# Optimization experiments

Measured on AMD Instinct MI355X. Metric: run time of the kernel, lower is better.

The kernel has to match this reference:

```python
import jax, jax.numpy as jnp
import numpy as np
import math

B, S, E, H = 2, 2048, 1024, 16
D = E // H
EPS = 1e-5


def setup_inputs() -> dict:
    key = jax.random.key(0)
    ks = jax.random.split(key, 6)
    s = 1.0 / math.sqrt(E)
    return {
        "query": jax.random.normal(ks[0], (B, S, E), jnp.float32),
        "Wq": jax.random.normal(ks[1], (E, E), jnp.float32) * s,
        "bq": jnp.zeros((E,), jnp.float32),
        "Wk": jax.random.normal(ks[2], (E, E), jnp.float32) * s,
        "bk": jnp.zeros((E,), jnp.float32),
        "Wv": jax.random.normal(ks[3], (E, E), jnp.float32) * s,
        "bv": jnp.zeros((E,), jnp.float32),
        "Wo": jax.random.normal(ks[4], (E, E), jnp.float32) * s,
        "bo": jnp.zeros((E,), jnp.float32),
        "alpha": jnp.ones((1,), jnp.float32),
    }


def reference(query, Wq, bq, Wk, bk, Wv, bv, Wo, bo, alpha):
    # Q/K/V projections (nn.Linear: x @ W.T + b)
    q = (query @ Wq.T + bq).reshape(B, S, H, D)
    k = (query @ Wk.T + bk).reshape(B, S, H, D)
    v = (query @ Wv.T + bv).reshape(B, S, H, D)

    # YAT scores: (q.k)^2 / (||q-k||^2 + eps)
    qk = jnp.einsum('bqhd,bkhd->bhqk', q, k)          # [B,H,S,S]
    sq = jnp.einsum('bqhd,bqhd->bhq', q, q)           # ||q||^2
    sk = jnp.einsum('bkhd,bkhd->bhk', k, k)           # ||k||^2
    dist_sq = sq[..., :, None] + sk[..., None, :] - 2.0 * qk
    scores = (qk * qk) / (dist_sq + EPS)

    # learnable alpha scaling: scores * (sqrt(d)/log(1+d))^alpha
    scale = (jnp.sqrt(jnp.float32(D)) / jnp.log1p(jnp.float32(D))) ** alpha[0]
    scores = scores * scale

    attn = jax.nn.softmax(scores, axis=-1)
    out = jnp.einsum('bhqk,bkhd->bqhd', attn, v).reshape(B, S, E)
    return out @ Wo.T + bo
```

## Files before the change

kernel.cpp:

```cpp
#include <hip/hip_runtime.h>
#include <hip/hip_fp16.h>
#include <math.h>

#define BB 2
#define SS 2048
#define EE 1024
#define HH 16
#define DD 64
#define YAT_EPS 1e-5f
#define RR (BB * HH * SS)

typedef __attribute__((ext_vector_type(8))) short bf16x8;
typedef __attribute__((ext_vector_type(4))) short short4v;
typedef __attribute__((ext_vector_type(4))) float f32x4;
#define MFMA16(a, b, c) __builtin_amdgcn_mfma_f32_16x16x32_bf16((a), (b), (c), 0, 0, 0)

#if __has_builtin(__builtin_amdgcn_exp2f)
#define EXP2(x) __builtin_amdgcn_exp2f(x)
#else
#define EXP2(x) exp2f(x)
#endif
#if __has_builtin(__builtin_amdgcn_rcpf)
#define RCPF(x) __builtin_amdgcn_rcpf(x)
#else
#define RCPF(x) (1.0f / (x))
#endif

__device__ __forceinline__ unsigned short f2bf(float x) {
    unsigned int u = __float_as_uint(x);
    u += 0x7FFFu + ((u >> 16) & 1u);
    return (unsigned short)(u >> 16);
}
__device__ __forceinline__ float bf2f(unsigned short h) {
    return __uint_as_float(((unsigned int)h) << 16);
}
__device__ __forceinline__ short f2bf_t(float x) {
    return (short)(__float_as_uint(x) >> 16);
}

__device__ __forceinline__ void async_ld16(void* lds, const void* g) {
    __builtin_amdgcn_global_load_lds(
        (const __attribute__((address_space(1))) unsigned int*)g,
        (__attribute__((address_space(3))) unsigned int*)lds, 16, 0, 0);
}

__global__ __launch_bounds__(256) void split_f32(const float* __restrict__ in,
                                                 unsigned short* __restrict__ hi,
                                                 unsigned short* __restrict__ lo,
                                                 int n4) {
    int i = blockIdx.x * 256 + threadIdx.x;
    if (i >= n4) return;
    float4 v = ((const float4*)in)[i];
    ushort4 h, l;
    h.x = f2bf(v.x); l.x = f2bf(v.x - bf2f(h.x));
    h.y = f2bf(v.y); l.y = f2bf(v.y - bf2f(h.y));
    h.z = f2bf(v.z); l.z = f2bf(v.z - bf2f(h.z));
    h.w = f2bf(v.w); l.w = f2bf(v.w - bf2f(h.w));
    ((ushort4*)hi)[i] = h;
    ((ushort4*)lo)[i] = l;
}

__global__ __launch_bounds__(256) void split_w4(
        const float* __restrict__ Wq, const float* __restrict__ Wk,
        const float* __restrict__ Wv, const float* __restrict__ Wo,
        unsigned short* __restrict__ Whi, unsigned short* __restrict__ Wlo,
        unsigned short* __restrict__ Wohi) {
    int i = blockIdx.x * 256 + threadIdx.x;
    int y = blockIdx.y;
    const float* src = y == 0 ? Wq : y == 1 ? Wk : y == 2 ? Wv : Wo;
    unsigned short* hi = y < 3 ? Whi + (size_t)y * EE * EE : Wohi;
    float4 v = ((const float4*)src)[i];
    ushort4 h;
    h.x = f2bf(v.x); h.y = f2bf(v.y); h.z = f2bf(v.z); h.w = f2bf(v.w);
    ((ushort4*)hi)[i] = h;
    if (y < 2) {
        unsigned short* lo = Wlo + (size_t)y * EE * EE;
        ushort4 l;
        l.x = f2bf(v.x - bf2f(h.x));
        l.y = f2bf(v.y - bf2f(h.y));
        l.z = f2bf(v.z - bf2f(h.z));
        l.w = f2bf(v.w - bf2f(h.w));
        ((ushort4*)lo)[i] = l;
    }
}

template <int MODE, int PASSES>
__global__ __launch_bounds__(256, 2) void gemm3p(
        const unsigned short* __restrict__ Ahi, const unsigned short* __restrict__ Alo,
        const unsigned short* __restrict__ Bhi, const unsigned short* __restrict__ Blo,
        const float* __restrict__ bq, const float* __restrict__ bk,
        const float* __restrict__ bv,
        float* __restrict__ Cf,
        unsigned short* __restrict__ qhi, unsigned short* __restrict__ qlo,
        unsigned short* __restrict__ khi,
        unsigned short* __restrict__ v_sd,
        float* __restrict__ sqn, float* __restrict__ skn,
        int M, int N, int K) {
    __shared__ __align__(16) unsigned short LA_hi[128 * 32];
    __shared__ __align__(16) unsigned short LA_lo[128 * 32];
    __shared__ __align__(16) unsigned short LB_hi[128 * 32];
    __shared__ __align__(16) unsigned short LB_lo[128 * 32];

    const int t = threadIdx.x;
    const int w = t >> 6, lane = t & 63;
    const int quad = lane >> 4, lr = lane & 15;
    const int wy = w & 1, wx = w >> 1;
    const int m0 = blockIdx.y * 128, n0 = blockIdx.x * 128;

    const unsigned short* gsrc = nullptr;
    unsigned short* ldst = nullptr;
    if (w == 0)      { gsrc = Ahi + (size_t)m0 * K; ldst = LA_hi; }
    else if (w == 2) { gsrc = Bhi + (size_t)n0 * K; ldst = LB_hi; }
    else if (PASSES == 3 && w == 1) { gsrc = Alo + (size_t)m0 * K; ldst = LA_lo; }
    else if (PASSES == 3 && w == 3) { gsrc = Blo + (size_t)n0 * K; ldst = LB_lo; }
    const unsigned short* gl = gsrc ? gsrc + (size_t)(lane >> 2) * K + (lane & 3) * 8
                                    : nullptr;

    f32x4 acc[4][4];
    #pragma unroll
    for (int i = 0; i < 4; ++i)
        #pragma unroll
        for (int j = 0; j < 4; ++j)
            acc[i][j] = (f32x4){0.f, 0.f, 0.f, 0.f};

    for (int k0 = 0; k0 < K; k0 += 32) {
        __syncthreads();
        if (gl) {
            #pragma unroll
            for (int i = 0; i < 8; ++i)
                async_ld16(ldst + i * 512, gl + (size_t)i * 16 * K + k0);
        }
        __syncthreads();
        bf16x8 ah[4], al[4], bh_[4], bl_[4];
        #pragma unroll
        for (int i = 0; i < 4; ++i) {
            ah[i]  = *(const bf16x8*)&LA_hi[(wy * 64 + i * 16 + lr) * 32 + quad * 8];
            bh_[i] = *(const bf16x8*)&LB_hi[(wx * 64 + i * 16 + lr) * 32 + quad * 8];
            if (PASSES == 3) {
                al[i]  = *(const bf16x8*)&LA_lo[(wy * 64 + i * 16 + lr) * 32 + quad * 8];
                bl_[i] = *(const bf16x8*)&LB_lo[(wx * 64 + i * 16 + lr) * 32 + quad * 8];
            }
        }
        #pragma unroll
        for (int mg = 0; mg < 4; ++mg)
            #pragma unroll
            for (int ns = 0; ns < 4; ++ns) {
                f32x4 a = acc[mg][ns];
                a = MFMA16(ah[mg], bh_[ns], a);
                if (PASSES == 3) {
                    a = MFMA16(ah[mg], bl_[ns], a);
                    a = MFMA16(al[mg], bh_[ns], a);
                }
                acc[mg][ns] = a;
            }
    }

    const int ng = n0 + wx * 64;
    if (MODE == 0) {
        float bias_v[4];
        #pragma unroll
        for (int ns = 0; ns < 4; ++ns) bias_v[ns] = bq[ng + ns * 16 + lr];
        #pragma unroll
        for (int mg = 0; mg < 4; ++mg)
            #pragma unroll
            for (int r = 0; r < 4; ++r) {
                int m = m0 + wy * 64 + mg * 16 + quad * 4 + r;
                #pragma unroll
                for (int ns = 0; ns < 4; ++ns)
                    Cf[(size_t)m * N + ng + ns * 16 + lr] = acc[mg][ns][r] + bias_v[ns];
            }
    } else {
        const int path = MODE == 1 ? (ng >> 10) : 2;
        const int c = MODE == 1 ? (ng & 1023) : ng;
        const int h = c >> 6;
        const float* bias = path == 0 ? bq : path == 1 ? bk : bv;
        unsigned short* hi_p = path == 0 ? qhi : path == 1 ? khi : v_sd;
        float* nrm = path == 0 ? sqn : skn;
        float bias_v[4];
        #pragma unroll
        for (int ns = 0; ns < 4; ++ns) bias_v[ns] = bias[c + ns * 16 + lr];
        #pragma unroll
        for (int mg = 0; mg < 4; ++mg)
            #pragma unroll
            for (int r = 0; r < 4; ++r) {
                int m = m0 + wy * 64 + mg * 16 + quad * 4 + r;
                int b = m >> 11, s = m & (SS - 1);
                size_t base = ((size_t)(b * HH + h) * SS + s) * DD;
                float v4[4];
                #pragma unroll
                for (int ns = 0; ns < 4; ++ns) v4[ns] = acc[mg][ns][r] + bias_v[ns];
                if (path < 2) {
                    float pn = v4[0] * v4[0] + v4[1] * v4[1] + v4[2] * v4[2] + v4[3] * v4[3];
                    #pragma unroll
                    for (int off = 1; off < 16; off <<= 1) pn += __shfl_xor(pn, off);
                    if (lr == 0) nrm[(size_t)(b * HH + h) * SS + s] = pn;
                    #pragma unroll
                    for (int ns = 0; ns < 4; ++ns) {
                        unsigned short hv = f2bf(v4[ns]);
                        hi_p[base + ns * 16 + lr] = hv;
                        if (path == 0)
                            qlo[base + ns * 16 + lr] = f2bf(v4[ns] - bf2f(hv));
                    }
                } else {
                    #pragma unroll
                    for (int ns = 0; ns < 4; ++ns)
                        hi_p[base + ns * 16 + lr] = f2bf(v4[ns]);
                }
            }
    }
}

__global__ __launch_bounds__(256) void transpose_v(const unsigned short* __restrict__ v_sd,
                                                   unsigned short* __restrict__ vt) {
    __shared__ unsigned short T[64][65];
    const int t = threadIdx.x;
    const int bh = blockIdx.y, s0 = blockIdx.x * 64;
    {
        int sl = t >> 2, d4 = (t & 3) * 16;
        const unsigned short* src = &v_sd[((size_t)bh * SS + s0 + sl) * DD + d4];
        bf16x8 a = *(const bf16x8*)src;
        bf16x8 b = *(const bf16x8*)(src + 8);
        #pragma unroll
        for (int j = 0; j < 8; ++j) {
            T[sl][d4 + j] = (unsigned short)a[j];
            T[sl][d4 + 8 + j] = (unsigned short)b[j];
        }
    }
    __syncthreads();
    {
        int dl = t >> 2, s4 = (t & 3) * 16;
        bf16x8 a, b;
        #pragma unroll
        for (int j = 0; j < 8; ++j) {
            a[j] = (short)T[s4 + j][dl];
            b[j] = (short)T[s4 + 8 + j][dl];
        }
        unsigned short* dst = &vt[((size_t)bh * DD + dl) * SS + s0 + s4];
        *(bf16x8*)dst = a;
        *(bf16x8*)(dst + 8) = b;
    }
}

__global__ __launch_bounds__(256, 3) void yat_attn_mfma(
        const unsigned short* __restrict__ qhi, const unsigned short* __restrict__ qlo,
        const unsigned short* __restrict__ khi,
        const unsigned short* __restrict__ vt,
        const float* __restrict__ sqn, const float* __restrict__ skn,
        const float* __restrict__ alphap,
        __half* __restrict__ Opart, float2* __restrict__ mlpart) {
    __shared__ __align__(16) unsigned short Ks[2][4096];
    __shared__ __align__(16) unsigned short Ps[2][4][16 * 68];

    const int t = threadIdx.x;
    const int w = t >> 6, lane = t & 63;
    const int quad = lane >> 4, lr = lane & 15;
    const int qt = blockIdx.x, bh = blockIdx.y, z = blockIdx.z;
    const int row0 = qt * 64 + w * 16;
    const float cscale = powf(sqrtf((float)DD) / log1pf((float)DD), alphap[0])
                         * 1.4426950408889634f;

    bf16x8 qh[2], ql[2];
    #pragma unroll
    for (int kd = 0; kd < 2; ++kd) {
        size_t o = ((size_t)bh * SS + row0 + lr) * DD + kd * 32 + quad * 8;
        qh[kd] = *(const bf16x8*)&qhi[o];
        ql[kd] = *(const bf16x8*)&qlo[o];
    }
    const float sqe = sqn[(size_t)bh * SS + row0 + lr] + YAT_EPS;

    const int lrow = lane >> 3;
    const int lofs = lrow * 64 + (((lane & 7) ^ (lrow & 7)) << 3);

    float m_r = -INFINITY, l_r = 0.f;
    f32x4 O[4];
    #pragma unroll
    for (int nd = 0; nd < 4; ++nd) O[nd] = (f32x4){0.f, 0.f, 0.f, 0.f};

    const int kt0 = z * 16;
    {
        const size_t gbase = ((size_t)bh * SS + kt0 * 64 + w * 16) * 64 + lofs;
        #pragma unroll
        for (int i2 = 0; i2 < 2; ++i2)
            async_ld16(&Ks[0][w * 1024 + i2 * 512], khi + gbase + i2 * 512);
    }

    for (int it = 0; it < 16; ++it) {
        const int kt = kt0 + it;
        const int p = it & 1;
        const int kbase = kt * 64;
        __syncthreads();
        if (it < 15) {
            const size_t gbase = ((size_t)bh * SS + (kt + 1) * 64 + w * 16) * 64 + lofs;
            #pragma unroll
            for (int i2 = 0; i2 < 2; ++i2)
                async_ld16(&Ks[p ^ 1][w * 1024 + i2 * 512], khi + gbase + i2 * 512);
        }
        f32x4 acc[4];
        f32x4 sk4[4];
        const unsigned short* kb = Ks[p];
        const int sw = lr & 7;
        #pragma unroll
        for (int st = 0; st < 4; ++st) {
            const int rbase = (st * 16 + lr) * 64;
            bf16x8 kh0 = *(const bf16x8*)&kb[rbase + ((quad    ) ^ sw) * 8];
            bf16x8 kh1 = *(const bf16x8*)&kb[rbase + ((quad + 4) ^ sw) * 8];
            sk4[st] = *(const f32x4*)&skn[(size_t)bh * SS + kbase + st * 16 + quad * 4];
            f32x4 a = (f32x4){0.f, 0.f, 0.f, 0.f};
            a = MFMA16(kh0, qh[0], a);
            a = MFMA16(kh1, qh[1], a);
            a = MFMA16(kh0, ql[0], a);
            a = MFMA16(kh1, ql[1], a);
            acc[st] = a;
        }
        bf16x8 vf[4][2];
        #pragma unroll
        for (int nd = 0; nd < 4; ++nd)
            #pragma unroll
            for (int kk = 0; kk < 2; ++kk)
                vf[nd][kk] = *(const bf16x8*)&vt[((size_t)bh * DD + nd * 16 + lr) * SS
                                                 + kbase + kk * 32 + quad * 8];
        unsigned short* myP = Ps[p][w];
        float mx = -INFINITY;
        #pragma unroll
        for (int st = 0; st < 4; ++st)
            #pragma unroll
            for (int r = 0; r < 4; ++r) {
                float qk = acc[st][r];
                float d = sqe + sk4[st][r] - 2.f * qk;
                float s = qk * qk * cscale * RCPF(d);
                acc[st][r] = s;
                mx = fmaxf(mx, s);
            }
        mx = fmaxf(mx, __shfl_xor(mx, 16));
        mx = fmaxf(mx, __shfl_xor(mx, 32));
        float mnew = fmaxf(m_r, mx);
        float aa = EXP2(m_r - mnew);
        m_r = mnew;
        float rs = 0.f;
        #pragma unroll
        for (int st = 0; st < 4; ++st)
            #pragma unroll
            for (int r = 0; r < 4; ++r) {
                float e = EXP2(acc[st][r] - mnew);
                acc[st][r] = e;
                rs += e;
            }
        rs += __shfl_xor(rs, 16);
        rs += __shfl_xor(rs, 32);
        l_r = l_r * aa + rs;
        #pragma unroll
        for (int st = 0; st < 4; ++st) {
            short4v pv;
            pv[0] = f2bf_t(acc[st][0]);
            pv[1] = f2bf_t(acc[st][1]);
            pv[2] = f2bf_t(acc[st][2]);
            pv[3] = f2bf_t(acc[st][3]);
            *(short4v*)&myP[lr * 68 + st * 16 + quad * 4] = pv;
        }
        float al_[4];
        #pragma unroll
        for (int r = 0; r < 4; ++r) al_[r] = __shfl(aa, quad * 4 + r);
        #pragma unroll
        for (int nd = 0; nd < 4; ++nd)
            #pragma unroll
            for (int r = 0; r < 4; ++r)
                O[nd][r] *= al_[r];
        bf16x8 pf[2];
        #pragma unroll
        for (int kk = 0; kk < 2; ++kk)
            pf[kk] = *(const bf16x8*)&myP[lr * 68 + kk * 32 + quad * 8];
        #pragma unroll
        for (int nd = 0; nd < 4; ++nd)
            #pragma unroll
            for (int kk = 0; kk < 2; ++kk)
                O[nd] = MFMA16(pf[kk], vf[nd][kk], O[nd]);
    }
    if (quad == 0)
        mlpart[(size_t)z * RR + (size_t)bh * SS + row0 + lr] = make_float2(m_r, l_r);
    #pragma unroll
    for (int r = 0; r < 4; ++r) {
        size_t rowg = (size_t)bh * SS + row0 + quad * 4 + r;
        #pragma unroll
        for (int nd = 0; nd < 4; ++nd)
            Opart[((size_t)z * RR + rowg) * DD + nd * 16 + lr] =
                __float2half(O[nd][r]);
    }
}

__global__ __launch_bounds__(256) void combine_attn(
        const __half* __restrict__ Opart, const float2* __restrict__ mlpart,
        unsigned short* __restrict__ ctxhi) {
    int tid = blockIdx.x * 256 + threadIdx.x;
    int row = tid >> 4, c4 = (tid & 15) * 4;
    float2 ml0 = mlpart[row];
    float2 ml1 = mlpart[RR + row];
    float ms = fmaxf(ml0.x, ml1.x);
    float a0 = EXP2(ml0.x - ms), a1 = EXP2(ml1.x - ms);
    float inv = RCPF(ml0.y * a0 + ml1.y * a1);
    a0 *= inv; a1 *= inv;
    const __half* p0 = Opart + (size_t)row * DD + c4;
    const __half* p1 = p0 + (size_t)RR * DD;
    int bh = row >> 11, s = row & (SS - 1);
    int b = bh >> 4, h = bh & 15;
    size_t idx = ((size_t)b * SS + s) * EE + h * DD + c4;
    ushort4 hv;
    unsigned short* hp = (unsigned short*)&hv;
    #pragma unroll
    for (int j = 0; j < 4; ++j) {
        float o = __half2float(p0[j]) * a0 + __half2float(p1[j]) * a1;
        hp[j] = f2bf(o);
    }
    *(ushort4*)&ctxhi[idx] = hv;
}

extern "C" void kernel_launch(void* const* d_in, const int* in_sizes, int n_in,
                              void* d_out, int out_size, void* d_ws, size_t ws_size,
                              hipStream_t stream) {
    const float* x     = (const float*)d_in[0];
    const float* Wq    = (const float*)d_in[1];
    const float* bq    = (const float*)d_in[2];
    const float* Wk    = (const float*)d_in[3];
    const float* bk    = (const float*)d_in[4];
    const float* Wv    = (const float*)d_in[5];
    const float* bv    = (const float*)d_in[6];
    const float* Wo    = (const float*)d_in[7];
    const float* bo    = (const float*)d_in[8];
    const float* alpha = (const float*)d_in[9];
    float* out = (float*)d_out;
    char* ws = (char*)d_ws;

    const int M = BB * SS;
    const size_t MB = 1u << 20;
    unsigned short* xhi  = (unsigned short*)(ws + 0 * MB);
    unsigned short* xlo  = (unsigned short*)(ws + 8 * MB);
    unsigned short* Whi  = (unsigned short*)(ws + 16 * MB);
    unsigned short* Wlo  = (unsigned short*)(ws + 22 * MB);
    unsigned short* vt   = (unsigned short*)(ws + 16 * MB);
    float2* mlpart       = (float2*)(ws + 24 * MB);
    unsigned short* Wohi = (unsigned short*)(ws + 28 * MB);
    unsigned short* qhi  = (unsigned short*)(ws + 32 * MB);
    unsigned short* qlo  = (unsigned short*)(ws + 40 * MB);
    unsigned short* khi  = (unsigned short*)(ws + 48 * MB);
    unsigned short* v_sd = (unsigned short*)(ws + 64 * MB);
    __half* Opart        = (__half*)(ws + 64 * MB);
    float* sqn = (float*)(ws + 80 * MB);
    float* skn = (float*)(ws + 80 * MB + 256 * 1024);
    unsigned short* ctxhi = xhi;

    const int nX = M * EE / 4, nW = EE * EE / 4;
    split_f32<<<nX / 256, 256, 0, stream>>>(x, xhi, xlo, nX);
    split_w4<<<dim3(nW / 256, 4), 256, 0, stream>>>(Wq, Wk, Wv, Wo, Whi, Wlo, Wohi);

    gemm3p<1, 3><<<dim3(2 * EE / 128, M / 128), 256, 0, stream>>>(
        xhi, xlo, Whi, Wlo, bq, bk, nullptr, nullptr,
        qhi, qlo, khi, nullptr, sqn, skn, M, 2 * EE, EE);
    gemm3p<2, 1><<<dim3(EE / 128, M / 128), 256, 0, stream>>>(
        xhi, nullptr, Whi + 2 * (size_t)EE * EE, nullptr, nullptr, nullptr, bv, nullptr,
        nullptr, nullptr, nullptr, v_sd, nullptr, nullptr, M, EE, EE);

    transpose_v<<<dim3(SS / 64, BB * HH), 256, 0, stream>>>(v_sd, vt);

    yat_attn_mfma<<<dim3(SS / 64, BB * HH, 2), 256, 0, stream>>>(
        qhi, qlo, khi, vt, sqn, skn, alpha, Opart, mlpart);

    combine_attn<<<RR * 16 / 256, 256, 0, stream>>>(Opart, mlpart, ctxhi);

    gemm3p<0, 1><<<dim3(EE / 128, M / 128), 256, 0, stream>>>(
        ctxhi, nullptr, Wohi, nullptr, bo, nullptr, nullptr, out,
        nullptr, nullptr, nullptr, nullptr, nullptr, nullptr, M, EE, EE);
}
```

Baseline: 358.1 us.

## Software-pipeline QK^T MFMA one key tile ahead of softmax

Restructures the attention loop so the Q·K score MFMAs for tile k+1 are issued before the YAT and softmax math for tile k, with K tiles prefetched two steps ahead into the double buffer. The goal is to overlap matrix-core work with the VALU-heavy score, exp and reduction phase and to hide LDS and global latency. It adds live registers (a second set of score accumulators and sk norms), which may lower occupancy or cause spills.

```diff
diff --git a/kernel.cpp b/kernel.cpp
--- a/kernel.cpp
+++ b/kernel.cpp
@@ -270,6 +270,7 @@
 
     const int lrow = lane >> 3;
     const int lofs = lrow * 64 + (((lane & 7) ^ (lrow & 7)) << 3);
+    const int sw = lr & 7;
 
     float m_r = -INFINITY, l_r = 0.f;
     f32x4 O[4];
@@ -277,40 +278,60 @@
     for (int nd = 0; nd < 4; ++nd) O[nd] = (f32x4){0.f, 0.f, 0.f, 0.f};
 
     const int kt0 = z * 16;
-    {
-        const size_t gbase = ((size_t)bh * SS + kt0 * 64 + w * 16) * 64 + lofs;
-        #pragma unroll
-        for (int i2 = 0; i2 < 2; ++i2)
-            async_ld16(&Ks[0][w * 1024 + i2 * 512], khi + gbase + i2 * 512);
+    const size_t khi_base = (size_t)bh * SS * 64 + (size_t)w * 16 * 64 + lofs;
+    const size_t skn_base = (size_t)bh * SS + quad * 4;
+
+    #pragma unroll
+    for (int i2 = 0; i2 < 2; ++i2)
+        async_ld16(&Ks[0][w * 1024 + i2 * 512],
+                   khi + khi_base + (size_t)(kt0 + 0) * 64 * 64 + i2 * 512);
+    __syncthreads();
+    #pragma unroll
+    for (int i2 = 0; i2 < 2; ++i2)
+        async_ld16(&Ks[1][w * 1024 + i2 * 512],
+                   khi + khi_base + (size_t)(kt0 + 1) * 64 * 64 + i2 * 512);
+
+    f32x4 accA[4], sk4A[4];
+    #pragma unroll
+    for (int st = 0; st < 4; ++st) {
+        const int rbase = (st * 16 + lr) * 64;
+        bf16x8 kh0 = *(const bf16x8*)&Ks[0][rbase + ((quad    ) ^ sw) * 8];
+        bf16x8 kh1 = *(const bf16x8*)&Ks[0][rbase + ((quad + 4) ^ sw) * 8];
+        sk4A[st] = *(const f32x4*)&skn[skn_base + (kt0 + 0) * 64 + st * 16];
+        f32x4 a = (f32x4){0.f, 0.f, 0.f, 0.f};
+        a = MFMA16(kh0, qh[0], a);
+        a = MFMA16(kh1, qh[1], a);
+        a = MFMA16(kh0, ql[0], a);
+        a = MFMA16(kh1, ql[1], a);
+        accA[st] = a;
     }
 
     for (int it = 0; it < 16; ++it) {
         const int kt = kt0 + it;
         const int p = it & 1;
-        const int kbase = kt * 64;
         __syncthreads();
-        if (it < 15) {
-            const size_t gbase = ((size_t)bh * SS + (kt + 1) * 64 + w * 16) * 64 + lofs;
+        if (it + 2 < 16) {
+            const size_t gb = khi_base + (size_t)(kt + 2) * 64 * 64;
             #pragma unroll
             for (int i2 = 0; i2 < 2; ++i2)
-                async_ld16(&Ks[p ^ 1][w * 1024 + i2 * 512], khi + gbase + i2 * 512);
-        }
-        f32x4 acc[4];
-        f32x4 sk4[4];
-        const unsigned short* kb = Ks[p];
-        const int sw = lr & 7;
-        #pragma unroll
-        for (int st = 0; st < 4; ++st) {
-            const int rbase = (st * 16 + lr) * 64;
-            bf16x8 kh0 = *(const bf16x8*)&kb[rbase + ((quad    ) ^ sw) * 8];
-            bf16x8 kh1 = *(const bf16x8*)&kb[rbase + ((quad + 4) ^ sw) * 8];
-            sk4[st] = *(const f32x4*)&skn[(size_t)bh * SS + kbase + st * 16 + quad * 4];
-            f32x4 a = (f32x4){0.f, 0.f, 0.f, 0.f};
-            a = MFMA16(kh0, qh[0], a);
-            a = MFMA16(kh1, qh[1], a);
-            a = MFMA16(kh0, ql[0], a);
-            a = MFMA16(kh1, ql[1], a);
-            acc[st] = a;
+                async_ld16(&Ks[p][w * 1024 + i2 * 512], khi + gb + i2 * 512);
+        }
+        f32x4 accB[4], sk4B[4];
+        if (it + 1 < 16) {
+            const unsigned short* kb = Ks[p ^ 1];
+            #pragma unroll
+            for (int st = 0; st < 4; ++st) {
+                const int rbase = (st * 16 + lr) * 64;
+                bf16x8 kh0 = *(const bf16x8*)&kb[rbase + ((quad    ) ^ sw) * 8];
+                bf16x8 kh1 = *(const bf16x8*)&kb[rbase + ((quad + 4) ^ sw) * 8];
+                sk4B[st] = *(const f32x4*)&skn[skn_base + (kt + 1) * 64 + st * 16];
+                f32x4 a = (f32x4){0.f, 0.f, 0.f, 0.f};
+                a = MFMA16(kh0, qh[0], a);
+                a = MFMA16(kh1, qh[1], a);
+                a = MFMA16(kh0, ql[0], a);
+                a = MFMA16(kh1, ql[1], a);
+                accB[st] = a;
+            }
         }
         bf16x8 vf[4][2];
         #pragma unroll
@@ -318,17 +339,17 @@
             #pragma unroll
             for (int kk = 0; kk < 2; ++kk)
                 vf[nd][kk] = *(const bf16x8*)&vt[((size_t)bh * DD + nd * 16 + lr) * SS
-                                                 + kbase + kk * 32 + quad * 8];
+                                                 + kt * 64 + kk * 32 + quad * 8];
         unsigned short* myP = Ps[p][w];
         float mx = -INFINITY;
         #pragma unroll
         for (int st = 0; st < 4; ++st)
             #pragma unroll
             for (int r = 0; r < 4; ++r) {
-                float qk = acc[st][r];
-                float d = sqe + sk4[st][r] - 2.f * qk;
+                float qk = accA[st][r];
+                float d = sqe + sk4A[st][r] - 2.f * qk;
                 float s = qk * qk * cscale * RCPF(d);
-                acc[st][r] = s;
+                accA[st][r] = s;
                 mx = fmaxf(mx, s);
             }
         mx = fmaxf(mx, __shfl_xor(mx, 16));
@@ -341,8 +362,8 @@
         for (int st = 0; st < 4; ++st)
             #pragma unroll
             for (int r = 0; r < 4; ++r) {
-                float e = EXP2(acc[st][r] - mnew);
-                acc[st][r] = e;
+                float e = EXP2(accA[st][r] - mnew);
+                accA[st][r] = e;
                 rs += e;
             }
         rs += __shfl_xor(rs, 16);
@@ -351,10 +372,10 @@
         #pragma unroll
         for (int st = 0; st < 4; ++st) {
             short4v pv;
-            pv[0] = f2bf_t(acc[st][0]);
-            pv[1] = f2bf_t(acc[st][1]);
-            pv[2] = f2bf_t(acc[st][2]);
-            pv[3] = f2bf_t(acc[st][3]);
+            pv[0] = f2bf_t(accA[st][0]);
+            pv[1] = f2bf_t(accA[st][1]);
+            pv[2] = f2bf_t(accA[st][2]);
+            pv[3] = f2bf_t(accA[st][3]);
             *(short4v*)&myP[lr * 68 + st * 16 + quad * 4] = pv;
         }
         float al_[4];
@@ -374,6 +395,8 @@
             #pragma unroll
             for (int kk = 0; kk < 2; ++kk)
                 O[nd] = MFMA16(pf[kk], vf[nd][kk], O[nd]);
+        #pragma unroll
+        for (int st = 0; st < 4; ++st) { accA[st] = accB[st]; sk4A[st] = sk4B[st]; }
     }
     if (quad == 0)
         mlpart[(size_t)z * RR + (size_t)bh * SS + row0 + lr] = make_float2(m_r, l_r);
```

Result: slower. 379.8 us (+6.1%).

## Drop split-K attention and combine kernel; fold scale into exp2 FMA

Applied to the files above, without the earlier changes.

Removes the two-way key split (z dimension) so each attention block walks all 32 key tiles and normalizes its own output, writing bf16 context directly and eliminating the combine_attn kernel plus the fp16 partial-output and max/sum round trip through memory. The score computation is restructured into paired float2 math, with the softmax scale applied inside the exp2 argument via an FMA instead of a per-element multiply. In exchange the attention grid halves to 1024 blocks, each doing twice the serial work, which reduces available parallelism and latency hiding.

```diff
diff --git a/kernel.cpp b/kernel.cpp
--- a/kernel.cpp
+++ b/kernel.cpp
@@ -1,5 +1,4 @@
 #include <hip/hip_runtime.h>
-#include <hip/hip_fp16.h>
 #include <math.h>
 
 #define BB 2
@@ -8,11 +7,11 @@
 #define HH 16
 #define DD 64
 #define YAT_EPS 1e-5f
-#define RR (BB * HH * SS)
 
 typedef __attribute__((ext_vector_type(8))) short bf16x8;
 typedef __attribute__((ext_vector_type(4))) short short4v;
 typedef __attribute__((ext_vector_type(4))) float f32x4;
+typedef __attribute__((ext_vector_type(2))) float f32x2;
 #define MFMA16(a, b, c) __builtin_amdgcn_mfma_f32_16x16x32_bf16((a), (b), (c), 0, 0, 0)
 
 #if __has_builtin(__builtin_amdgcn_exp2f)
@@ -247,14 +246,15 @@
         const unsigned short* __restrict__ vt,
         const float* __restrict__ sqn, const float* __restrict__ skn,
         const float* __restrict__ alphap,
-        __half* __restrict__ Opart, float2* __restrict__ mlpart) {
+        unsigned short* __restrict__ ctxhi) {
     __shared__ __align__(16) unsigned short Ks[2][4096];
     __shared__ __align__(16) unsigned short Ps[2][4][16 * 68];
 
     const int t = threadIdx.x;
     const int w = t >> 6, lane = t & 63;
     const int quad = lane >> 4, lr = lane & 15;
-    const int qt = blockIdx.x, bh = blockIdx.y, z = blockIdx.z;
+    const int qt = blockIdx.x, bh = blockIdx.y;
+    const int b = bh >> 4, h = bh & 15;
     const int row0 = qt * 64 + w * 16;
     const float cscale = powf(sqrtf((float)DD) / log1pf((float)DD), alphap[0])
                          * 1.4426950408889634f;
@@ -270,41 +270,40 @@
 
     const int lrow = lane >> 3;
     const int lofs = lrow * 64 + (((lane & 7) ^ (lrow & 7)) << 3);
+    const int sw = lr & 7;
 
     float m_r = -INFINITY, l_r = 0.f;
     f32x4 O[4];
     #pragma unroll
     for (int nd = 0; nd < 4; ++nd) O[nd] = (f32x4){0.f, 0.f, 0.f, 0.f};
 
-    const int kt0 = z * 16;
+    const size_t khi_base = (size_t)bh * SS * 64 + (size_t)w * 16 * 64 + lofs;
+    const size_t skn_base = (size_t)bh * SS + quad * 4;
+
     {
-        const size_t gbase = ((size_t)bh * SS + kt0 * 64 + w * 16) * 64 + lofs;
         #pragma unroll
         for (int i2 = 0; i2 < 2; ++i2)
-            async_ld16(&Ks[0][w * 1024 + i2 * 512], khi + gbase + i2 * 512);
-    }
-
-    for (int it = 0; it < 16; ++it) {
-        const int kt = kt0 + it;
+            async_ld16(&Ks[0][w * 1024 + i2 * 512], khi + khi_base + i2 * 512);
+    }
+
+    for (int it = 0; it < SS / 64; ++it) {
         const int p = it & 1;
-        const int kbase = kt * 64;
         __syncthreads();
-        if (it < 15) {
-            const size_t gbase = ((size_t)bh * SS + (kt + 1) * 64 + w * 16) * 64 + lofs;
+        if (it + 1 < SS / 64) {
+            const size_t gb = khi_base + (size_t)(it + 1) * 64 * 64;
             #pragma unroll
             for (int i2 = 0; i2 < 2; ++i2)
-                async_ld16(&Ks[p ^ 1][w * 1024 + i2 * 512], khi + gbase + i2 * 512);
+                async_ld16(&Ks[p ^ 1][w * 1024 + i2 * 512], khi + gb + i2 * 512);
         }
         f32x4 acc[4];
         f32x4 sk4[4];
         const unsigned short* kb = Ks[p];
-        const int sw = lr & 7;
         #pragma unroll
         for (int st = 0; st < 4; ++st) {
             const int rbase = (st * 16 + lr) * 64;
             bf16x8 kh0 = *(const bf16x8*)&kb[rbase + ((quad    ) ^ sw) * 8];
             bf16x8 kh1 = *(const bf16x8*)&kb[rbase + ((quad + 4) ^ sw) * 8];
-            sk4[st] = *(const f32x4*)&skn[(size_t)bh * SS + kbase + st * 16 + quad * 4];
+            sk4[st] = *(const f32x4*)&skn[skn_base + it * 64 + st * 16];
             f32x4 a = (f32x4){0.f, 0.f, 0.f, 0.f};
             a = MFMA16(kh0, qh[0], a);
             a = MFMA16(kh1, qh[1], a);
@@ -318,45 +317,45 @@
             #pragma unroll
             for (int kk = 0; kk < 2; ++kk)
                 vf[nd][kk] = *(const bf16x8*)&vt[((size_t)bh * DD + nd * 16 + lr) * SS
-                                                 + kbase + kk * 32 + quad * 8];
-        unsigned short* myP = Ps[p][w];
+                                                 + it * 64 + kk * 32 + quad * 8];
+        f32x2 U[8];
+        const f32x2 sq2 = (f32x2){sqe, sqe};
         float mx = -INFINITY;
         #pragma unroll
         for (int st = 0; st < 4; ++st)
             #pragma unroll
-            for (int r = 0; r < 4; ++r) {
-                float qk = acc[st][r];
-                float d = sqe + sk4[st][r] - 2.f * qk;
-                float s = qk * qk * cscale * RCPF(d);
-                acc[st][r] = s;
-                mx = fmaxf(mx, s);
+            for (int pr = 0; pr < 2; ++pr) {
+                f32x2 qk = (f32x2){acc[st][pr * 2], acc[st][pr * 2 + 1]};
+                f32x2 skp = (f32x2){sk4[st][pr * 2], sk4[st][pr * 2 + 1]};
+                f32x2 dd = sq2 + skp - (qk + qk);
+                f32x2 rr = (f32x2){RCPF(dd.x), RCPF(dd.y)};
+                f32x2 uu = qk * qk * rr;
+                U[st * 2 + pr] = uu;
+                mx = fmaxf(mx, fmaxf(uu.x, uu.y));
             }
         mx = fmaxf(mx, __shfl_xor(mx, 16));
         mx = fmaxf(mx, __shfl_xor(mx, 32));
         float mnew = fmaxf(m_r, mx);
-        float aa = EXP2(m_r - mnew);
+        float cm = cscale * mnew;
+        float aa = EXP2(__builtin_fmaf(cscale, m_r, -cm));
         m_r = mnew;
+        unsigned short* myP = Ps[p][w];
         float rs = 0.f;
         #pragma unroll
-        for (int st = 0; st < 4; ++st)
-            #pragma unroll
-            for (int r = 0; r < 4; ++r) {
-                float e = EXP2(acc[st][r] - mnew);
-                acc[st][r] = e;
-                rs += e;
-            }
+        for (int st = 0; st < 4; ++st) {
+            float e0 = EXP2(__builtin_fmaf(cscale, U[st * 2].x,     -cm));
+            float e1 = EXP2(__builtin_fmaf(cscale, U[st * 2].y,     -cm));
+            float e2 = EXP2(__builtin_fmaf(cscale, U[st * 2 + 1].x, -cm));
+            float e3 = EXP2(__builtin_fmaf(cscale, U[st * 2 + 1].y, -cm));
+            rs += (e0 + e1) + (e2 + e3);
+            short4v pv;
+            pv[0] = f2bf_t(e0); pv[1] = f2bf_t(e1);
+            pv[2] = f2bf_t(e2); pv[3] = f2bf_t(e3);
+            *(short4v*)&myP[lr * 68 + st * 16 + quad * 4] = pv;
+        }
         rs += __shfl_xor(rs, 16);
         rs += __shfl_xor(rs, 32);
         l_r = l_r * aa + rs;
-        #pragma unroll
-        for (int st = 0; st < 4; ++st) {
-            short4v pv;
-            pv[0] = f2bf_t(acc[st][0]);
-            pv[1] = f2bf_t(acc[st][1]);
-            pv[2] = f2bf_t(acc[st][2]);
-            pv[3] = f2bf_t(acc[st][3]);
-            *(short4v*)&myP[lr * 68 + st * 16 + quad * 4] = pv;
-        }
         float al_[4];
         #pragma unroll
         for (int r = 0; r < 4; ++r) al_[r] = __shfl(aa, quad * 4 + r);
@@ -375,42 +374,17 @@
             for (int kk = 0; kk < 2; ++kk)
                 O[nd] = MFMA16(pf[kk], vf[nd][kk], O[nd]);
     }
-    if (quad == 0)
-        mlpart[(size_t)z * RR + (size_t)bh * SS + row0 + lr] = make_float2(m_r, l_r);
+    float linv[4];
+    #pragma unroll
+    for (int r = 0; r < 4; ++r) linv[r] = RCPF(__shfl(l_r, quad * 4 + r));
     #pragma unroll
     for (int r = 0; r < 4; ++r) {
-        size_t rowg = (size_t)bh * SS + row0 + quad * 4 + r;
+        int row = row0 + quad * 4 + r;
         #pragma unroll
         for (int nd = 0; nd < 4; ++nd)
-            Opart[((size_t)z * RR + rowg) * DD + nd * 16 + lr] =
-                __float2half(O[nd][r]);
-    }
-}
-
-__global__ __launch_bounds__(256) void combine_attn(
-        const __half* __restrict__ Opart, const float2* __restrict__ mlpart,
-        unsigned short* __restrict__ ctxhi) {
-    int tid = blockIdx.x * 256 + threadIdx.x;
-    int row = tid >> 4, c4 = (tid & 15) * 4;
-    float2 ml0 = mlpart[row];
-    float2 ml1 = mlpart[RR + row];
-    float ms = fmaxf(ml0.x, ml1.x);
-    float a0 = EXP2(ml0.x - ms), a1 = EXP2(ml1.x - ms);
-    float inv = RCPF(ml0.y * a0 + ml1.y * a1);
-    a0 *= inv; a1 *= inv;
-    const __half* p0 = Opart + (size_t)row * DD + c4;
-    const __half* p1 = p0 + (size_t)RR * DD;
-    int bh = row >> 11, s = row & (SS - 1);
-    int b = bh >> 4, h = bh & 15;
-    size_t idx = ((size_t)b * SS + s) * EE + h * DD + c4;
-    ushort4 hv;
-    unsigned short* hp = (unsigned short*)&hv;
-    #pragma unroll
-    for (int j = 0; j < 4; ++j) {
-        float o = __half2float(p0[j]) * a0 + __half2float(p1[j]) * a1;
-        hp[j] = f2bf(o);
-    }
-    *(ushort4*)&ctxhi[idx] = hv;
+            ctxhi[((size_t)b * SS + row) * EE + h * DD + nd * 16 + lr] =
+                f2bf(O[nd][r] * linv[r]);
+    }
 }
 
 extern "C" void kernel_launch(void* const* d_in, const int* in_sizes, int n_in,
@@ -436,13 +410,11 @@
     unsigned short* Whi  = (unsigned short*)(ws + 16 * MB);
     unsigned short* Wlo  = (unsigned short*)(ws + 22 * MB);
     unsigned short* vt   = (unsigned short*)(ws + 16 * MB);
-    float2* mlpart       = (float2*)(ws + 24 * MB);
     unsigned short* Wohi = (unsigned short*)(ws + 28 * MB);
     unsigned short* qhi  = (unsigned short*)(ws + 32 * MB);
     unsigned short* qlo  = (unsigned short*)(ws + 40 * MB);
     unsigned short* khi  = (unsigned short*)(ws + 48 * MB);
     unsigned short* v_sd = (unsigned short*)(ws + 64 * MB);
-    __half* Opart        = (__half*)(ws + 64 * MB);
     float* sqn = (float*)(ws + 80 * MB);
     float* skn = (float*)(ws + 80 * MB + 256 * 1024);
     unsigned short* ctxhi = xhi;
@@ -460,10 +432,8 @@
 
     transpose_v<<<dim3(SS / 64, BB * HH), 256, 0, stream>>>(v_sd, vt);
 
-    yat_attn_mfma<<<dim3(SS / 64, BB * HH, 2), 256, 0, stream>>>(
-        qhi, qlo, khi, vt, sqn, skn, alpha, Opart, mlpart);
-
-    combine_attn<<<RR * 16 / 256, 256, 0, stream>>>(Opart, mlpart, ctxhi);
+    yat_attn_mfma<<<dim3(SS / 64, BB * HH), 256, 0, stream>>>(
+        qhi, qlo, khi, vt, sqn, skn, alpha, ctxhi);
 
     gemm3p<0, 1><<<dim3(EE / 128, M / 128), 256, 0, stream>>>(
         ctxhi, nullptr, Wohi, nullptr, bo, nullptr, nullptr, out,
```

After: 384.3 us. 7.3% more time.

## Stage two 64-key K tiles per barrier and fold score scale into exp FMA

Applied to the files above, without the earlier changes.

The K double buffer now holds 128 keys per stage, so each barrier and async prefetch covers two 64-key subtiles processed back to back. This halves the number of __syncthreads and prefetch issues per block. The score scale is also moved out of the per-element score computation: the running max is kept unscaled and the scale is applied through an FMA inside the exp2 argument, with the stored max rescaled at the end. The larger K buffer raises LDS use per block, which could limit how many blocks fit on a CU.

```diff
diff --git a/kernel.cpp b/kernel.cpp
--- a/kernel.cpp
+++ b/kernel.cpp
@@ -248,7 +248,7 @@
         const float* __restrict__ sqn, const float* __restrict__ skn,
         const float* __restrict__ alphap,
         __half* __restrict__ Opart, float2* __restrict__ mlpart) {
-    __shared__ __align__(16) unsigned short Ks[2][4096];
+    __shared__ __align__(16) unsigned short Ks[2][8192];
     __shared__ __align__(16) unsigned short Ps[2][4][16 * 68];
 
     const int t = threadIdx.x;
@@ -270,113 +270,119 @@
 
     const int lrow = lane >> 3;
     const int lofs = lrow * 64 + (((lane & 7) ^ (lrow & 7)) << 3);
+    const int sw = lr & 15 & 7;
 
     float m_r = -INFINITY, l_r = 0.f;
     f32x4 O[4];
     #pragma unroll
     for (int nd = 0; nd < 4; ++nd) O[nd] = (f32x4){0.f, 0.f, 0.f, 0.f};
 
-    const int kt0 = z * 16;
-    {
-        const size_t gbase = ((size_t)bh * SS + kt0 * 64 + w * 16) * 64 + lofs;
+    const int t0 = z * 16;
+    const size_t khi_base = (size_t)bh * SS * 64 + (size_t)w * 16 * 64 + lofs;
+    const size_t skn_base = (size_t)bh * SS + quad * 4;
+
+    #pragma unroll
+    for (int tl = 0; tl < 2; ++tl)
         #pragma unroll
         for (int i2 = 0; i2 < 2; ++i2)
-            async_ld16(&Ks[0][w * 1024 + i2 * 512], khi + gbase + i2 * 512);
-    }
-
-    for (int it = 0; it < 16; ++it) {
-        const int kt = kt0 + it;
+            async_ld16(&Ks[0][tl * 4096 + w * 1024 + i2 * 512],
+                       khi + khi_base + (size_t)(t0 + tl) * 4096 + i2 * 512);
+
+    for (int it = 0; it < 8; ++it) {
         const int p = it & 1;
-        const int kbase = kt * 64;
         __syncthreads();
-        if (it < 15) {
-            const size_t gbase = ((size_t)bh * SS + (kt + 1) * 64 + w * 16) * 64 + lofs;
-            #pragma unroll
-            for (int i2 = 0; i2 < 2; ++i2)
-                async_ld16(&Ks[p ^ 1][w * 1024 + i2 * 512], khi + gbase + i2 * 512);
-        }
-        f32x4 acc[4];
-        f32x4 sk4[4];
-        const unsigned short* kb = Ks[p];
-        const int sw = lr & 7;
-        #pragma unroll
-        for (int st = 0; st < 4; ++st) {
-            const int rbase = (st * 16 + lr) * 64;
-            bf16x8 kh0 = *(const bf16x8*)&kb[rbase + ((quad    ) ^ sw) * 8];
-            bf16x8 kh1 = *(const bf16x8*)&kb[rbase + ((quad + 4) ^ sw) * 8];
-            sk4[st] = *(const f32x4*)&skn[(size_t)bh * SS + kbase + st * 16 + quad * 4];
-            f32x4 a = (f32x4){0.f, 0.f, 0.f, 0.f};
-            a = MFMA16(kh0, qh[0], a);
-            a = MFMA16(kh1, qh[1], a);
-            a = MFMA16(kh0, ql[0], a);
-            a = MFMA16(kh1, ql[1], a);
-            acc[st] = a;
-        }
-        bf16x8 vf[4][2];
-        #pragma unroll
-        for (int nd = 0; nd < 4; ++nd)
+        if (it + 1 < 8) {
+            #pragma unroll
+            for (int tl = 0; tl < 2; ++tl)
+                #pragma unroll
+                for (int i2 = 0; i2 < 2; ++i2)
+                    async_ld16(&Ks[p ^ 1][tl * 4096 + w * 1024 + i2 * 512],
+                               khi + khi_base
+                                   + (size_t)(t0 + 2 * (it + 1) + tl) * 4096
+                                   + i2 * 512);
+        }
+        #pragma unroll
+        for (int sub = 0; sub < 2; ++sub) {
+            const int kbase = (t0 + 2 * it + sub) * 64;
+            const unsigned short* kb = &Ks[p][sub * 4096];
+            f32x4 acc[4];
+            f32x4 sk4[4];
+            #pragma unroll
+            for (int st = 0; st < 4; ++st) {
+                const int rbase = (st * 16 + lr) * 64;
+                bf16x8 kh0 = *(const bf16x8*)&kb[rbase + ((quad    ) ^ sw) * 8];
+                bf16x8 kh1 = *(const bf16x8*)&kb[rbase + ((quad + 4) ^ sw) * 8];
+                sk4[st] = *(const f32x4*)&skn[skn_base + kbase + st * 16];
+                f32x4 a = (f32x4){0.f, 0.f, 0.f, 0.f};
+                a = MFMA16(kh0, qh[0], a);
+                a = MFMA16(kh1, qh[1], a);
+                a = MFMA16(kh0, ql[0], a);
+                a = MFMA16(kh1, ql[1], a);
+                acc[st] = a;
+            }
+            bf16x8 vf[4][2];
+            #pragma unroll
+            for (int nd = 0; nd < 4; ++nd)
+                #pragma unroll
+                for (int kk = 0; kk < 2; ++kk)
+                    vf[nd][kk] = *(const bf16x8*)&vt[((size_t)bh * DD + nd * 16 + lr) * SS
+                                                     + kbase + kk * 32 + quad * 8];
+            float mx = -INFINITY;
+            #pragma unroll
+            for (int st = 0; st < 4; ++st)
+                #pragma unroll
+                for (int r = 0; r < 4; ++r) {
+                    float qk = acc[st][r];
+                    float d = sqe + sk4[st][r] - 2.f * qk;
+                    float u = qk * qk * RCPF(d);
+                    acc[st][r] = u;
+                    mx = fmaxf(mx, u);
+                }
+            mx = fmaxf(mx, __shfl_xor(mx, 16));
+            mx = fmaxf(mx, __shfl_xor(mx, 32));
+            float mnew = fmaxf(m_r, mx);
+            float cm = cscale * mnew;
+            float aa = EXP2(__builtin_fmaf(cscale, m_r, -cm));
+            m_r = mnew;
+            unsigned short* myP = Ps[p][w];
+            float rs = 0.f;
+            #pragma unroll
+            for (int st = 0; st < 4; ++st) {
+                float e0 = EXP2(__builtin_fmaf(cscale, acc[st][0], -cm));
+                float e1 = EXP2(__builtin_fmaf(cscale, acc[st][1], -cm));
+                float e2 = EXP2(__builtin_fmaf(cscale, acc[st][2], -cm));
+                float e3 = EXP2(__builtin_fmaf(cscale, acc[st][3], -cm));
+                rs += (e0 + e1) + (e2 + e3);
+                short4v pv;
+                pv[0] = f2bf_t(e0); pv[1] = f2bf_t(e1);
+                pv[2] = f2bf_t(e2); pv[3] = f2bf_t(e3);
+                *(short4v*)&myP[lr * 68 + st * 16 + quad * 4] = pv;
+            }
+            rs += __shfl_xor(rs, 16);
+            rs += __shfl_xor(rs, 32);
+            l_r = l_r * aa + rs;
+            float al_[4];
+            #pragma unroll
+            for (int r = 0; r < 4; ++r) al_[r] = __shfl(aa, quad * 4 + r);
+            #pragma unroll
+            for (int nd = 0; nd < 4; ++nd)
+                #pragma unroll
+                for (int r = 0; r < 4; ++r)
+                    O[nd][r] *= al_[r];
+            bf16x8 pf[2];
             #pragma unroll
             for (int kk = 0; kk < 2; ++kk)
-                vf[nd][kk] = *(const bf16x8*)&vt[((size_t)bh * DD + nd * 16 + lr) * SS
-                                                 + kbase + kk * 32 + quad * 8];
-        unsigned short* myP = Ps[p][w];
-        float mx = -INFINITY;
-        #pragma unroll
-        for (int st = 0; st < 4; ++st)
-            #pragma unroll
-            for (int r = 0; r < 4; ++r) {
-                float qk = acc[st][r];
-                float d = sqe + sk4[st][r] - 2.f * qk;
-                float s = qk * qk * cscale * RCPF(d);
-                acc[st][r] = s;
-                mx = fmaxf(mx, s);
-            }
-        mx = fmaxf(mx, __shfl_xor(mx, 16));
-        mx = fmaxf(mx, __shfl_xor(mx, 32));
-        float mnew = fmaxf(m_r, mx);
-        float aa = EXP2(m_r - mnew);
-        m_r = mnew;
-        float rs = 0.f;
-        #pragma unroll
-        for (int st = 0; st < 4; ++st)
-            #pragma unroll
-            for (int r = 0; r < 4; ++r) {
-                float e = EXP2(acc[st][r] - mnew);
-                acc[st][r] = e;
-                rs += e;
-            }
-        rs += __shfl_xor(rs, 16);
-        rs += __shfl_xor(rs, 32);
-        l_r = l_r * aa + rs;
-        #pragma unroll
-        for (int st = 0; st < 4; ++st) {
-            short4v pv;
-            pv[0] = f2bf_t(acc[st][0]);
-            pv[1] = f2bf_t(acc[st][1]);
-            pv[2] = f2bf_t(acc[st][2]);
-            pv[3] = f2bf_t(acc[st][3]);
-            *(short4v*)&myP[lr * 68 + st * 16 + quad * 4] = pv;
-        }
-        float al_[4];
-        #pragma unroll
-        for (int r = 0; r < 4; ++r) al_[r] = __shfl(aa, quad * 4 + r);
-        #pragma unroll
-        for (int nd = 0; nd < 4; ++nd)
-            #pragma unroll
-            for (int r = 0; r < 4; ++r)
-                O[nd][r] *= al_[r];
-        bf16x8 pf[2];
-        #pragma unroll
-        for (int kk = 0; kk < 2; ++kk)
-            pf[kk] = *(const bf16x8*)&myP[lr * 68 + kk * 32 + quad * 8];
-        #pragma unroll
-        for (int nd = 0; nd < 4; ++nd)
-            #pragma unroll
-            for (int kk = 0; kk < 2; ++kk)
-                O[nd] = MFMA16(pf[kk], vf[nd][kk], O[nd]);
+                pf[kk] = *(const bf16x8*)&myP[lr * 68 + kk * 32 + quad * 8];
+            #pragma unroll
+            for (int nd = 0; nd < 4; ++nd)
+                #pragma unroll
+                for (int kk = 0; kk < 2; ++kk)
+                    O[nd] = MFMA16(pf[kk], vf[nd][kk], O[nd]);
+        }
     }
     if (quad == 0)
-        mlpart[(size_t)z * RR + (size_t)bh * SS + row0 + lr] = make_float2(m_r, l_r);
+        mlpart[(size_t)z * RR + (size_t)bh * SS + row0 + lr] =
+            make_float2(cscale * m_r, l_r);
     #pragma unroll
     for (int r = 0; r < 4; ++r) {
         size_t rowg = (size_t)bh * SS + row0 + quad * 4 + r;
```

Measured after the change: 357.3 us. Within noise of the previous version (-0.2%).
